# Performance work log

Measured on AMD Instinct MI355X. Metric: run time of the kernel, lower is better.

## Reference

```python
import jax, jax.numpy as jnp
import numpy as np

B, T, N, D = 4, 12, 512, 128
L = 4            # max_lag + 1 lag encoders
H = D // 2       # lag-encoder hidden dim
THRESHOLD = 0.1


def setup_inputs() -> dict:
    key = jax.random.key(0)
    ks = jax.random.split(key, 10)
    s = 0.02
    return {
        "x":   jax.random.normal(ks[0], (B, T, N, D), dtype=jnp.float32),
        # lag encoders: Linear(D->H), ReLU, Linear(H->D), stacked over L lags
        "W1":  s * jax.random.normal(ks[1], (L, D, H), dtype=jnp.float32),
        "b1":  jnp.zeros((L, H), dtype=jnp.float32),
        "W2":  s * jax.random.normal(ks[2], (L, H, D), dtype=jnp.float32),
        "b2":  jnp.zeros((L, D), dtype=jnp.float32),
        # causal scorer: Linear(2D->D), ReLU, (Dropout=id in eval), Linear(D->1), Sigmoid
        "Ws1": s * jax.random.normal(ks[3], (2 * D, D), dtype=jnp.float32),
        "bs1": jnp.zeros((D,), dtype=jnp.float32),
        "Ws2": s * jax.random.normal(ks[4], (D, 1), dtype=jnp.float32),
        "bs2": jnp.zeros((1,), dtype=jnp.float32),
    }


def reference(x, W1, b1, W2, b2, Ws1, bs1, Ws2, bs2):
    Tdim = x.shape[1]
    # lagged slices x[:, T-1-lag] for lag in 0..L-1 (all lags active since T > max_lag)
    lags = jnp.stack([x[:, max(0, Tdim - 1 - l)] for l in range(L)], axis=1)  # (B,L,N,D)
    h = jax.nn.relu(jnp.einsum('blnd,ldh->blnh', lags, W1) + b1[None, :, None, :])
    enc = jnp.einsum('blnh,lhd->blnd', h, W2) + b2[None, :, None, :]          # (B,L,N,D)
    agg = enc.mean(axis=1)                                                    # (B,N,D)

    # pairwise causal scorer. cat([src, tgt]) @ Ws1 == src @ Ws1[:D] + tgt @ Ws1[D:],
    # avoiding the explicit (B,N,N,2D) concat.
    src_proj = jnp.einsum('bnd,dk->bnk', agg, Ws1[:D])   # (B,N,D)
    tgt_proj = jnp.einsum('bnd,dk->bnk', agg, Ws1[D:])   # (B,N,D)
    pre = src_proj[:, :, None, :] + tgt_proj[:, None, :, :] + bs1  # (B,N,N,D)
    score = jax.nn.sigmoid(jnp.einsum('bijd,d->bij', jax.nn.relu(pre), Ws2[:, 0]) + bs2[0])

    # threshold sparsification + remove self loops
    adj = jnp.where(score > THRESHOLD, score, 0.0)
    adj = adj * (1.0 - jnp.eye(N, dtype=adj.dtype))

    # multi-hop propagation and global max normalization per batch element
    a2 = jnp.matmul(adj, adj)
    a3 = jnp.matmul(a2, adj)
    enhanced = adj + 0.5 * a2 + 0.25 * a3
    mx = jnp.max(enhanced, axis=(-1, -2), keepdims=True)
    return enhanced / (mx + 1e-8)
```

## Files before the change

kernel.cpp:

```cpp
#include <hip/hip_runtime.h>
#include <math.h>

#define Bn 4
#define Tn 12
#define Nn 512
#define Dn 128
#define Ln 4
#define Hn 64
#define NNe (Nn*Nn)

typedef __attribute__((ext_vector_type(8))) short short8;
typedef __attribute__((ext_vector_type(4))) float f32x4;

__device__ __forceinline__ unsigned short f2bf(float f) {
    unsigned int u = __float_as_uint(f);
    unsigned int r = (u + 0x7FFF + ((u >> 16) & 1)) >> 16;
    return (unsigned short)r;
}
__device__ __forceinline__ float bf2f(unsigned short s) {
    return __uint_as_float(((unsigned int)s) << 16);
}

__global__ __launch_bounds__(256) void k_enc_a(
    const float* __restrict__ x, const float* __restrict__ W1, const float* __restrict__ b1,
    unsigned short* __restrict__ hb, unsigned int* __restrict__ maxslot)
{
    __shared__ __align__(16) unsigned short xA[32*136];
    __shared__ __align__(16) unsigned short w1T[64*136];
    int tid = threadIdx.x;
    int rg = blockIdx.x, lag = blockIdx.y;
    if (rg == 0 && lag == 0 && tid < Bn) maxslot[tid] = 0u;
    int r0 = rg * 32;
    int bb = r0 >> 9, n0 = r0 & 511;

    {
        const float4* xs = (const float4*)(x + ((size_t)(bb*Tn + (Tn-1-lag))*Nn + n0)*Dn);
        for (int v = tid; v < 1024; v += 256) {
            float4 f = xs[v];
            int row = v >> 5, c4 = v & 31;
            ushort4 o = { f2bf(f.x), f2bf(f.y), f2bf(f.z), f2bf(f.w) };
            *(ushort4*)&xA[row*136 + c4*4] = o;
        }
    }
    {
        int n = tid & 63, kq = tid >> 6;
        const float* Wp = W1 + (size_t)lag*Dn*Hn;
        #pragma unroll
        for (int r = 0; r < 4; ++r) {
            int k0 = (r*4 + kq)*8;
            unsigned short tmp[8];
            #pragma unroll
            for (int j = 0; j < 8; ++j) tmp[j] = f2bf(Wp[(size_t)(k0+j)*Hn + n]);
            *(short8*)&w1T[n*136 + k0] = *(const short8*)tmp;
        }
    }
    __syncthreads();

    int wv = __builtin_amdgcn_readfirstlane(tid >> 6);
    int lane = tid & 63;
    int wm = wv >> 1, wn = wv & 1;
    int m = lane & 15, q = lane >> 4;
    f32x4 acc[2] = {{0.f,0.f,0.f,0.f},{0.f,0.f,0.f,0.f}};
    #pragma unroll
    for (int ks = 0; ks < 4; ++ks) {
        short8 af = *(const short8*)&xA[(wm*16 + m)*136 + ks*32 + q*8];
        #pragma unroll
        for (int nt = 0; nt < 2; ++nt) {
            short8 bg = *(const short8*)&w1T[(wn*32 + nt*16 + m)*136 + ks*32 + q*8];
            acc[nt] = __builtin_amdgcn_mfma_f32_16x16x32_bf16(af, bg, acc[nt], 0, 0, 0);
        }
    }
    int colL = lane & 15, rq = lane >> 4;
    #pragma unroll
    for (int nt = 0; nt < 2; ++nt) {
        int ncol = wn*32 + nt*16 + colL;
        float bv = b1[lag*Hn + ncol];
        #pragma unroll
        for (int reg = 0; reg < 4; ++reg) {
            int rowL = wm*16 + rq*4 + reg;
            hb[(size_t)(r0+rowL)*256 + lag*64 + ncol] = f2bf(fmaxf(acc[nt][reg] + bv, 0.f));
        }
    }
}

__global__ __launch_bounds__(256) void k_enc_bc(
    const unsigned short* __restrict__ hb, const float* __restrict__ W2,
    const float* __restrict__ b2, const float* __restrict__ Ws1,
    const float* __restrict__ bs1,
    unsigned short* __restrict__ spb, unsigned short* __restrict__ tpb)
{
    __shared__ __align__(16) unsigned short hA[16*264];
    __shared__ __align__(16) unsigned short wT[64*264];
    __shared__ __align__(16) unsigned short aggA[16*136];
    int tid = threadIdx.x;
    int wv = __builtin_amdgcn_readfirstlane(tid >> 6);
    int lane = tid & 63;
    int r0 = blockIdx.x * 16;

    for (int v = tid; v < 512; v += 256) {
        int row = v >> 5, c = v & 31;
        *(short8*)&hA[row*264 + c*8] = *(const short8*)(hb + (size_t)(r0+row)*256 + c*8);
    }

    int m = lane & 15, q = lane >> 4;
    int colL = lane & 15, rq = lane >> 4;

    for (int ch = 0; ch < 2; ++ch) {
        __syncthreads();
        {
            int n = tid & 63, kq = tid >> 6;
            #pragma unroll
            for (int r = 0; r < 8; ++r) {
                int k0 = (r*4 + kq)*8;
                unsigned short tmp[8];
                #pragma unroll
                for (int j = 0; j < 8; ++j) tmp[j] = f2bf(W2[(size_t)(k0+j)*Dn + ch*64 + n]);
                *(short8*)&wT[n*264 + k0] = *(const short8*)tmp;
            }
        }
        __syncthreads();
        f32x4 acc = {0.f,0.f,0.f,0.f};
        #pragma unroll
        for (int ks = 0; ks < 8; ++ks) {
            short8 af = *(const short8*)&hA[m*264 + ks*32 + q*8];
            short8 bg = *(const short8*)&wT[(wv*16 + m)*264 + ks*32 + q*8];
            acc = __builtin_amdgcn_mfma_f32_16x16x32_bf16(af, bg, acc, 0, 0, 0);
        }
        int col = ch*64 + wv*16 + colL;
        float b2s = b2[col] + b2[Dn+col] + b2[2*Dn+col] + b2[3*Dn+col];
        #pragma unroll
        for (int reg = 0; reg < 4; ++reg)
            aggA[(rq*4+reg)*136 + col] = f2bf(0.25f*(acc[reg] + b2s));
    }

    for (int tgt = 0; tgt < 2; ++tgt) {
        __syncthreads();
        {
            int n = tid & 127, kq = tid >> 7;
            #pragma unroll
            for (int r = 0; r < 8; ++r) {
                int k0 = (r*2 + kq)*8;
                unsigned short tmp[8];
                #pragma unroll
                for (int j = 0; j < 8; ++j)
                    tmp[j] = f2bf(Ws1[(size_t)(tgt*Dn + k0 + j)*Dn + n]);
                *(short8*)&wT[n*136 + k0] = *(const short8*)tmp;
            }
        }
        __syncthreads();
        f32x4 acc[2] = {{0.f,0.f,0.f,0.f},{0.f,0.f,0.f,0.f}};
        #pragma unroll
        for (int ks = 0; ks < 4; ++ks) {
            short8 af = *(const short8*)&aggA[m*136 + ks*32 + q*8];
            #pragma unroll
            for (int nt = 0; nt < 2; ++nt) {
                short8 bg = *(const short8*)&wT[(wv*32 + nt*16 + m)*136 + ks*32 + q*8];
                acc[nt] = __builtin_amdgcn_mfma_f32_16x16x32_bf16(af, bg, acc[nt], 0, 0, 0);
            }
        }
        unsigned short* dst = tgt ? tpb : spb;
        #pragma unroll
        for (int nt = 0; nt < 2; ++nt) {
            int n = wv*32 + nt*16 + colL;
            float bv = tgt ? 0.f : bs1[n];
            #pragma unroll
            for (int reg = 0; reg < 4; ++reg)
                dst[(size_t)(r0 + rq*4 + reg)*Dn + n] = f2bf(acc[nt][reg] + bv);
        }
    }
}

__global__ __launch_bounds__(256) void k_score(
    const unsigned short* __restrict__ spb, const unsigned short* __restrict__ tpb,
    const float* __restrict__ Ws2, const float* __restrict__ bs2,
    unsigned short* __restrict__ adj_b, unsigned short* __restrict__ adj_bt)
{
    __shared__ float spl[64*132];
    __shared__ unsigned short tplT[Dn*72];
    int tid = threadIdx.x;
    int wv = __builtin_amdgcn_readfirstlane(tid >> 6);
    int lane = tid & 63;
    int bz = blockIdx.z;
    int i0b = blockIdx.y * 64, j0b = blockIdx.x * 64;
    const unsigned short* spr = spb + (size_t)bz*Nn*Dn;
    const unsigned short* tpr = tpb + (size_t)bz*Nn*Dn;

    for (int v = tid; v < 1024; v += 256) {
        int row = v >> 4, c = v & 15;
        const unsigned short* src = spr + (size_t)(i0b+row)*Dn + c*8;
        ushort4 u0 = *(const ushort4*)src;
        ushort4 u1 = *(const ushort4*)(src + 4);
        float4 f0 = { bf2f(u0.x), bf2f(u0.y), bf2f(u0.z), bf2f(u0.w) };
        float4 f1 = { bf2f(u1.x), bf2f(u1.y), bf2f(u1.z), bf2f(u1.w) };
        *(float4*)&spl[row*132 + c*8]     = f0;
        *(float4*)&spl[row*132 + c*8 + 4] = f1;
    }
    {
        int j = tid & 63, kq = tid >> 6;
        for (int p = 0; p < 4; ++p) {
            int k8 = p*4 + kq;
            short8 tv = *(const short8*)(tpr + (size_t)(j0b+j)*Dn + k8*8);
            #pragma unroll
            for (int t = 0; t < 8; ++t) tplT[(k8*8+t)*72 + j] = (unsigned short)tv[t];
        }
    }
    __syncthreads();

    int iq = lane >> 4, jq = lane & 15;
    int iw = wv*16 + iq*4;
    float acc[4][4] = {};
    for (int k8 = 0; k8 < 16; ++k8) {
        float4 wa = *(const float4*)(Ws2 + k8*8);
        float4 wb = *(const float4*)(Ws2 + k8*8 + 4);
        float4 sA[4], sB[4];
        #pragma unroll
        for (int ii = 0; ii < 4; ++ii) {
            sA[ii] = *(const float4*)&spl[(iw+ii)*132 + k8*8];
            sB[ii] = *(const float4*)&spl[(iw+ii)*132 + k8*8 + 4];
        }
        ushort4 t4[8];
        #pragma unroll
        for (int kk = 0; kk < 8; ++kk) t4[kk] = *(const ushort4*)&tplT[(k8*8+kk)*72 + jq*4];
        #pragma unroll
        for (int kk = 0; kk < 8; ++kk) {
            float w = (kk < 4) ? ((const float*)&wa)[kk] : ((const float*)&wb)[kk-4];
            float tv0 = bf2f(t4[kk].x), tv1 = bf2f(t4[kk].y);
            float tv2 = bf2f(t4[kk].z), tv3 = bf2f(t4[kk].w);
            #pragma unroll
            for (int ii = 0; ii < 4; ++ii) {
                float s = (kk < 4) ? ((const float*)&sA[ii])[kk] : ((const float*)&sB[ii])[kk-4];
                acc[ii][0] += fmaxf(s + tv0, 0.f)*w;
                acc[ii][1] += fmaxf(s + tv1, 0.f)*w;
                acc[ii][2] += fmaxf(s + tv2, 0.f)*w;
                acc[ii][3] += fmaxf(s + tv3, 0.f)*w;
            }
        }
    }
    float bsv = bs2[0];
    int i0 = i0b + iw;
    int j0 = j0b + jq*4;
    float vals[4][4];
    #pragma unroll
    for (int ii = 0; ii < 4; ++ii) {
        int i = i0 + ii;
        #pragma unroll
        for (int jj = 0; jj < 4; ++jj) {
            float z = acc[ii][jj] + bsv;
            float sc = 1.f/(1.f + __expf(-z));
            int j = j0 + jj;
            vals[ii][jj] = (sc > 0.1f && i != j) ? sc : 0.f;
        }
    }
    size_t base = (size_t)bz << 18;
    #pragma unroll
    for (int ii = 0; ii < 4; ++ii) {
        ushort4 rv = make_ushort4(f2bf(vals[ii][0]), f2bf(vals[ii][1]),
                                  f2bf(vals[ii][2]), f2bf(vals[ii][3]));
        *(ushort4*)(adj_b + base + (size_t)(i0+ii)*Nn + j0) = rv;
    }
    #pragma unroll
    for (int jj = 0; jj < 4; ++jj) {
        ushort4 cv = make_ushort4(f2bf(vals[0][jj]), f2bf(vals[1][jj]),
                                  f2bf(vals[2][jj]), f2bf(vals[3][jj]));
        *(ushort4*)(adj_bt + base + (size_t)(j0+jj)*Nn + i0) = cv;
    }
}

__global__ __launch_bounds__(256) void k_mm1(
    const unsigned short* __restrict__ adj_b, const unsigned short* __restrict__ adj_bt,
    unsigned short* __restrict__ a2b)
{
    __shared__ unsigned short Als[64*72];
    __shared__ unsigned short Bls[64*72];
    int tid = threadIdx.x;
    int wv = __builtin_amdgcn_readfirstlane(tid >> 6);
    int lane = tid & 63;
    int b = blockIdx.z, i0 = blockIdx.y*64, j0 = blockIdx.x*64;
    size_t base = (size_t)b << 18;
    const unsigned short* Ab = adj_b + base;
    const unsigned short* Bb = adj_bt + base;
    int wm = wv >> 1, wn = wv & 1;
    int m = lane & 15, q = lane >> 4;
    int sr = tid >> 2, sc = (tid & 3)*16;
    f32x4 acc[2][2];
    #pragma unroll
    for (int mt = 0; mt < 2; ++mt)
        #pragma unroll
        for (int nt = 0; nt < 2; ++nt) acc[mt][nt] = (f32x4){0.f,0.f,0.f,0.f};
    short8 pa0, pa1, pb0, pb1;
    pa0 = *(const short8*)(Ab + (size_t)(i0+sr)*Nn + sc);
    pa1 = *(const short8*)(Ab + (size_t)(i0+sr)*Nn + sc + 8);
    pb0 = *(const short8*)(Bb + (size_t)(j0+sr)*Nn + sc);
    pb1 = *(const short8*)(Bb + (size_t)(j0+sr)*Nn + sc + 8);
    for (int kt = 0; kt < 8; ++kt) {
        *(short8*)&Als[sr*72 + sc]     = pa0;
        *(short8*)&Als[sr*72 + sc + 8] = pa1;
        *(short8*)&Bls[sr*72 + sc]     = pb0;
        *(short8*)&Bls[sr*72 + sc + 8] = pb1;
        __syncthreads();
        if (kt < 7) {
            int k0 = (kt+1)*64;
            pa0 = *(const short8*)(Ab + (size_t)(i0+sr)*Nn + k0 + sc);
            pa1 = *(const short8*)(Ab + (size_t)(i0+sr)*Nn + k0 + sc + 8);
            pb0 = *(const short8*)(Bb + (size_t)(j0+sr)*Nn + k0 + sc);
            pb1 = *(const short8*)(Bb + (size_t)(j0+sr)*Nn + k0 + sc + 8);
        }
        #pragma unroll
        for (int ks = 0; ks < 2; ++ks) {
            short8 af[2], bg[2];
            #pragma unroll
            for (int mt = 0; mt < 2; ++mt) af[mt] = *(const short8*)&Als[(wm*32+mt*16+m)*72 + ks*32 + q*8];
            #pragma unroll
            for (int nt = 0; nt < 2; ++nt) bg[nt] = *(const short8*)&Bls[(wn*32+nt*16+m)*72 + ks*32 + q*8];
            #pragma unroll
            for (int mt = 0; mt < 2; ++mt)
                #pragma unroll
                for (int nt = 0; nt < 2; ++nt)
                    acc[mt][nt] = __builtin_amdgcn_mfma_f32_16x16x32_bf16(af[mt], bg[nt], acc[mt][nt], 0, 0, 0);
        }
        __syncthreads();
    }
    int col = lane & 15, rq = lane >> 4;
    #pragma unroll
    for (int mt = 0; mt < 2; ++mt)
        #pragma unroll
        for (int nt = 0; nt < 2; ++nt)
            #pragma unroll
            for (int reg = 0; reg < 4; ++reg) {
                int i = i0 + wm*32 + mt*16 + rq*4 + reg;
                int j = j0 + wn*32 + nt*16 + col;
                a2b[base + (size_t)i*Nn + j] = f2bf(acc[mt][nt][reg]);
            }
}

__global__ __launch_bounds__(256) void k_mm2(
    const unsigned short* __restrict__ adj_b, const unsigned short* __restrict__ adj_bt,
    const unsigned short* __restrict__ a2b,
    float* __restrict__ out, unsigned int* __restrict__ maxslot)
{
    __shared__ unsigned short Als[64*72];
    __shared__ unsigned short Bls[64*72];
    __shared__ float red[4];
    int tid = threadIdx.x;
    int wv = __builtin_amdgcn_readfirstlane(tid >> 6);
    int lane = tid & 63;
    int b = blockIdx.z, i0 = blockIdx.y*64, j0 = blockIdx.x*64;
    size_t base = (size_t)b << 18;
    const unsigned short* Ab = a2b + base;
    const unsigned short* Bb = adj_bt + base;
    int wm = wv >> 1, wn = wv & 1;
    int m = lane & 15, q = lane >> 4;
    int sr = tid >> 2, sc = (tid & 3)*16;
    f32x4 acc[2][2];
    #pragma unroll
    for (int mt = 0; mt < 2; ++mt)
        #pragma unroll
        for (int nt = 0; nt < 2; ++nt) acc[mt][nt] = (f32x4){0.f,0.f,0.f,0.f};
    short8 pa0, pa1, pb0, pb1;
    pa0 = *(const short8*)(Ab + (size_t)(i0+sr)*Nn + sc);
    pa1 = *(const short8*)(Ab + (size_t)(i0+sr)*Nn + sc + 8);
    pb0 = *(const short8*)(Bb + (size_t)(j0+sr)*Nn + sc);
    pb1 = *(const short8*)(Bb + (size_t)(j0+sr)*Nn + sc + 8);
    for (int kt = 0; kt < 8; ++kt) {
        *(short8*)&Als[sr*72 + sc]     = pa0;
        *(short8*)&Als[sr*72 + sc + 8] = pa1;
        *(short8*)&Bls[sr*72 + sc]     = pb0;
        *(short8*)&Bls[sr*72 + sc + 8] = pb1;
        __syncthreads();
        if (kt < 7) {
            int k0 = (kt+1)*64;
            pa0 = *(const short8*)(Ab + (size_t)(i0+sr)*Nn + k0 + sc);
            pa1 = *(const short8*)(Ab + (size_t)(i0+sr)*Nn + k0 + sc + 8);
            pb0 = *(const short8*)(Bb + (size_t)(j0+sr)*Nn + k0 + sc);
            pb1 = *(const short8*)(Bb + (size_t)(j0+sr)*Nn + k0 + sc + 8);
        }
        #pragma unroll
        for (int ks = 0; ks < 2; ++ks) {
            short8 af[2], bg[2];
            #pragma unroll
            for (int mt = 0; mt < 2; ++mt) af[mt] = *(const short8*)&Als[(wm*32+mt*16+m)*72 + ks*32 + q*8];
            #pragma unroll
            for (int nt = 0; nt < 2; ++nt) bg[nt] = *(const short8*)&Bls[(wn*32+nt*16+m)*72 + ks*32 + q*8];
            #pragma unroll
            for (int mt = 0; mt < 2; ++mt)
                #pragma unroll
                for (int nt = 0; nt < 2; ++nt)
                    acc[mt][nt] = __builtin_amdgcn_mfma_f32_16x16x32_bf16(af[mt], bg[nt], acc[mt][nt], 0, 0, 0);
        }
        __syncthreads();
    }
    int col = lane & 15, rq = lane >> 4;
    float lmax = 0.f;
    const unsigned short* adjp = adj_b + base;
    #pragma unroll
    for (int mt = 0; mt < 2; ++mt)
        #pragma unroll
        for (int nt = 0; nt < 2; ++nt)
            #pragma unroll
            for (int reg = 0; reg < 4; ++reg) {
                int i = i0 + wm*32 + mt*16 + rq*4 + reg;
                int j = j0 + wn*32 + nt*16 + col;
                size_t off = (size_t)i*Nn + j;
                float e = bf2f(adjp[off]) + 0.5f*bf2f(Ab[off]) + 0.25f*acc[mt][nt][reg];
                out[base + off] = e;
                lmax = fmaxf(lmax, e);
            }
    #pragma unroll
    for (int s = 1; s < 64; s <<= 1) lmax = fmaxf(lmax, __shfl_xor(lmax, s, 64));
    if (lane == 0) red[wv] = lmax;
    __syncthreads();
    if (tid == 0) {
        float mx = fmaxf(fmaxf(red[0], red[1]), fmaxf(red[2], red[3]));
        atomicMax(maxslot + b, __float_as_uint(mx));
    }
}

__global__ __launch_bounds__(256) void k_norm(float* __restrict__ out,
                                              const unsigned int* __restrict__ maxslot)
{
    int idx = blockIdx.x*256 + threadIdx.x;
    int b = idx >> 16;
    float m = __uint_as_float(maxslot[b]);
    float inv = 1.f/(m + 1e-8f);
    float4* p = (float4*)out + idx;
    float4 v = *p;
    v.x *= inv; v.y *= inv; v.z *= inv; v.w *= inv;
    *p = v;
}

extern "C" void kernel_launch(void* const* d_in, const int* in_sizes, int n_in,
                              void* d_out, int out_size, void* d_ws, size_t ws_size,
                              hipStream_t stream) {
    const float* x   = (const float*)d_in[0];
    const float* W1  = (const float*)d_in[1];
    const float* b1  = (const float*)d_in[2];
    const float* W2  = (const float*)d_in[3];
    const float* b2  = (const float*)d_in[4];
    const float* Ws1 = (const float*)d_in[5];
    const float* bs1 = (const float*)d_in[6];
    const float* Ws2 = (const float*)d_in[7];
    const float* bs2 = (const float*)d_in[8];
    float* out = (float*)d_out;

    unsigned char* wsb = (unsigned char*)d_ws;
    unsigned short* spb    = (unsigned short*)(wsb);
    unsigned short* tpb    = (unsigned short*)(wsb + (512u<<10));
    unsigned short* adj_b  = (unsigned short*)(wsb + (1024u<<10));
    unsigned short* adj_bt = (unsigned short*)(wsb + (3072u<<10));
    unsigned short* a2b    = (unsigned short*)(wsb + (5120u<<10));
    unsigned int*   maxslot= (unsigned int*)(wsb + (7168u<<10));
    unsigned short* hb     = (unsigned short*)(wsb + (7172u<<10));

    k_enc_a <<<dim3(64, 4),   256, 0, stream>>>(x, W1, b1, hb, maxslot);
    k_enc_bc<<<dim3(128),     256, 0, stream>>>(hb, W2, b2, Ws1, bs1, spb, tpb);
    k_score <<<dim3(8, 8, Bn),256, 0, stream>>>(spb, tpb, Ws2, bs2, adj_b, adj_bt);
    k_mm1   <<<dim3(8, 8, Bn),256, 0, stream>>>(adj_b, adj_bt, a2b);
    k_mm2   <<<dim3(8, 8, Bn),256, 0, stream>>>(adj_b, adj_bt, a2b, out, maxslot);
    k_norm  <<<dim3(1024),    256, 0, stream>>>(out, maxslot);
}
```

Measured before the change: 123.2 us.

## Fuse max normalization into final matmul via grid-wide spin barrier

Removes the separate normalization kernel. The final matmul kernel now keeps its enhanced values in registers, increments a global counter, and spins until all 256 blocks have posted their per-batch max. It then writes the already-normalized output directly. This avoids one kernel launch and a full read-modify-write pass over the 4 MB output, but it relies on all 256 blocks being co-resident, otherwise the spin will deadlock.

```diff
diff --git a/kernel.cpp b/kernel.cpp
--- a/kernel.cpp
+++ b/kernel.cpp
@@ -29,7 +29,7 @@
     __shared__ __align__(16) unsigned short w1T[64*136];
     int tid = threadIdx.x;
     int rg = blockIdx.x, lag = blockIdx.y;
-    if (rg == 0 && lag == 0 && tid < Bn) maxslot[tid] = 0u;
+    if (rg == 0 && lag == 0 && tid < 8) maxslot[tid] = 0u;
     int r0 = rg * 32;
     int bb = r0 >> 9, n0 = r0 & 511;
 
@@ -341,6 +341,7 @@
     __shared__ unsigned short Als[64*72];
     __shared__ unsigned short Bls[64*72];
     __shared__ float red[4];
+    __shared__ float gmax;
     int tid = threadIdx.x;
     int wv = __builtin_amdgcn_readfirstlane(tid >> 6);
     int lane = tid & 63;
@@ -391,6 +392,7 @@
     }
     int col = lane & 15, rq = lane >> 4;
     float lmax = 0.f;
+    float e[2][2][4];
     const unsigned short* adjp = adj_b + base;
     #pragma unroll
     for (int mt = 0; mt < 2; ++mt)
@@ -401,31 +403,35 @@
                 int i = i0 + wm*32 + mt*16 + rq*4 + reg;
                 int j = j0 + wn*32 + nt*16 + col;
                 size_t off = (size_t)i*Nn + j;
-                float e = bf2f(adjp[off]) + 0.5f*bf2f(Ab[off]) + 0.25f*acc[mt][nt][reg];
-                out[base + off] = e;
-                lmax = fmaxf(lmax, e);
+                float v = bf2f(adjp[off]) + 0.5f*bf2f(Ab[off]) + 0.25f*acc[mt][nt][reg];
+                e[mt][nt][reg] = v;
+                lmax = fmaxf(lmax, v);
             }
     #pragma unroll
     for (int s = 1; s < 64; s <<= 1) lmax = fmaxf(lmax, __shfl_xor(lmax, s, 64));
     if (lane == 0) red[wv] = lmax;
     __syncthreads();
+    unsigned int* cnt = maxslot + 4;
     if (tid == 0) {
         float mx = fmaxf(fmaxf(red[0], red[1]), fmaxf(red[2], red[3]));
         atomicMax(maxslot + b, __float_as_uint(mx));
-    }
-}
-
-__global__ __launch_bounds__(256) void k_norm(float* __restrict__ out,
-                                              const unsigned int* __restrict__ maxslot)
-{
-    int idx = blockIdx.x*256 + threadIdx.x;
-    int b = idx >> 16;
-    float m = __uint_as_float(maxslot[b]);
-    float inv = 1.f/(m + 1e-8f);
-    float4* p = (float4*)out + idx;
-    float4 v = *p;
-    v.x *= inv; v.y *= inv; v.z *= inv; v.w *= inv;
-    *p = v;
+        __threadfence();
+        atomicAdd(cnt, 1u);
+        while (atomicAdd(cnt, 0u) < 256u) __builtin_amdgcn_s_sleep(16);
+        gmax = __uint_as_float(atomicMax(maxslot + b, 0u));
+    }
+    __syncthreads();
+    float inv = 1.f/(gmax + 1e-8f);
+    #pragma unroll
+    for (int mt = 0; mt < 2; ++mt)
+        #pragma unroll
+        for (int nt = 0; nt < 2; ++nt)
+            #pragma unroll
+            for (int reg = 0; reg < 4; ++reg) {
+                int i = i0 + wm*32 + mt*16 + rq*4 + reg;
+                int j = j0 + wn*32 + nt*16 + col;
+                out[base + (size_t)i*Nn + j] = e[mt][nt][reg]*inv;
+            }
 }
 
 extern "C" void kernel_launch(void* const* d_in, const int* in_sizes, int n_in,
@@ -456,5 +462,4 @@
     k_score <<<dim3(8, 8, Bn),256, 0, stream>>>(spb, tpb, Ws2, bs2, adj_b, adj_bt);
     k_mm1   <<<dim3(8, 8, Bn),256, 0, stream>>>(adj_b, adj_bt, a2b);
     k_mm2   <<<dim3(8, 8, Bn),256, 0, stream>>>(adj_b, adj_bt, a2b, out, maxslot);
-    k_norm  <<<dim3(1024),    256, 0, stream>>>(out, maxslot);
-}
+}
```

Result: slower. 127.6 us (+3.6%).
